# Optimization experiments

Measured on AMD Instinct MI355X. Metric: run time of the kernel, lower is better.

Reference implementation:

```python
import jax, jax.numpy as jnp
import numpy as np

B, L, D = 4, 4096, 1024
H, M = 16, 256
DH = D // H  # 64


def setup_inputs() -> dict:
    key = jax.random.key(0)
    ks = jax.random.split(key, 7)
    s = 1.0 / np.sqrt(D).astype(np.float32)  # keep activations O(1) so exp() stays sane
    x = jax.random.normal(ks[0], (B, L, D), dtype=jnp.float32)
    Wq = jax.random.normal(ks[1], (D, D), dtype=jnp.float32) * s
    Wk = jax.random.normal(ks[2], (D, D), dtype=jnp.float32) * s
    Wv = jax.random.normal(ks[3], (D, D), dtype=jnp.float32) * s
    Wo = jax.random.normal(ks[4], (D, D), dtype=jnp.float32) * s
    bo = jnp.zeros((D,), dtype=jnp.float32)
    omega = jax.random.normal(ks[5], (DH, M), dtype=jnp.float32)
    return {"x": x, "Wq": Wq, "Wk": Wk, "Wv": Wv, "Wo": Wo, "bo": bo, "omega": omega}


def _phi(x, omega):
    # x: (B,H,L,dh) -> positive random features (B,H,L,m)
    scale = DH ** 0.25
    x_s = x / scale
    proj = jnp.einsum('bhld,dm->bhlm', x_s, omega)
    norm_sq = jnp.sum(x_s * x_s, axis=-1, keepdims=True) * 0.5
    return jnp.exp(proj - norm_sq) / (M ** 0.5)


def reference(x, Wq, Wk, Wv, Wo, bo, omega):
    # nn.Linear: y = x @ W.T
    def heads(W):
        return (x @ W.T).reshape(B, L, H, DH).transpose(0, 2, 1, 3)
    Q, K, V = heads(Wq), heads(Wk), heads(Wv)
    Q_feat = _phi(Q, omega)   # (B,H,L,m)
    K_feat = _phi(K, omega)   # (B,H,L,m)
    KV = jnp.einsum('bhlm,bhld->bhmd', K_feat, V)      # (B,H,m,dh)
    out = jnp.einsum('bhlm,bhmd->bhld', Q_feat, KV)    # (B,H,L,dh)
    K_sum = K_feat.sum(axis=2)                          # (B,H,m)
    norm = jnp.einsum('bhlm,bhm->bhl', Q_feat, K_sum)
    norm = jnp.clip(norm, 1e-6, None)[..., None]
    out = out / norm
    out = out.transpose(0, 2, 1, 3).reshape(B, L, D)
    return out @ Wo.T + bo
```

## Files before the change

### kernel.cpp

```cpp
#include <hip/hip_runtime.h>

typedef unsigned short u16;
typedef __attribute__((ext_vector_type(4))) float f32x4;
typedef _Float16 f16x8 __attribute__((ext_vector_type(8)));
typedef __attribute__((ext_vector_type(4))) u16   u16x4;
typedef __attribute__((ext_vector_type(8))) u16   u16x8;

#define DEV static __device__ __forceinline__

constexpr int Ll = 4096;

DEV float h2f(u16 v) { _Float16 h; __builtin_memcpy(&h, &v, 2); return (float)h; }
DEV u16 f2h(float f) { _Float16 h = (_Float16)f; u16 u; __builtin_memcpy(&u, &h, 2); return u; }

DEV f32x4 mfma16h(f16x8 a, f16x8 b, f32x4 c) {
    return __builtin_amdgcn_mfma_f32_16x16x32_f16(a, b, c, 0, 0, 0);
}

#if defined(__has_builtin)
#if __has_builtin(__builtin_amdgcn_global_load_lds)
#define HAS_GLLDS 1
#endif
#endif
#ifndef HAS_GLLDS
#define HAS_GLLDS 0
#endif

#if HAS_GLLDS
#define STG(BUF, U, SRC, ROWBASE, KK)                                                \
  { int rl_ = wave * 16 + (lane >> 2);                                               \
    int c_ = lane & 3;                                                               \
    int grow_ = (((U) & 1) * 128) + rl_;                                             \
    const u16* gp_ = (SRC) + (size_t)((ROWBASE) + grow_) * 1024 + (KK)               \
                     + ((c_ ^ ((rl_ >> 1) & 3)) * 8);                                \
    __builtin_amdgcn_global_load_lds(                                                \
        (const __attribute__((address_space(1))) unsigned int*)gp_,                  \
        (__attribute__((address_space(3))) unsigned int*)(sm + (BUF) * 16384 +       \
            (U) * 4096 + wave * 512), 16, 0, 0); }
#else
#define STG(BUF, U, SRC, ROWBASE, KK)                                                \
  { int rl_ = wave * 16 + (lane >> 2);                                               \
    int c_ = lane & 3;                                                               \
    int grow_ = (((U) & 1) * 128) + rl_;                                             \
    const u16* gp_ = (SRC) + (size_t)((ROWBASE) + grow_) * 1024 + (KK)               \
                     + ((c_ ^ ((rl_ >> 1) & 3)) * 8);                                \
    *(u16x8*)(sm + (BUF) * 16384 + (U) * 4096 + wave * 512 + lane * 8)               \
        = *(const u16x8*)gp_; }
#endif

__global__ __launch_bounds__(256) void k_half(const float* __restrict__ s, u16* __restrict__ d) {
    size_t i = ((size_t)blockIdx.x * 256 + threadIdx.x) * 4;
    f32x4 v = *(const f32x4*)(s + i);
    u16x4 h;
#pragma unroll
    for (int j = 0; j < 4; j++) h[j] = f2h(v[j]);
    *(u16x4*)(d + i) = h;
}

__global__ __launch_bounds__(256) void k_omega(const float* __restrict__ om, u16* __restrict__ wh) {
    int i = blockIdx.x * 256 + threadIdx.x;
    int m = i >> 6, d = i & 63;
    wh[i] = f2h(om[d * 256 + m] * 0.35355339059327373f);
}

__global__ __launch_bounds__(256) void k_zero(float* __restrict__ p, int n) {
    int i = (blockIdx.x * 256 + threadIdx.x) * 4;
    if (i < n) { f32x4 z; z[0]=0.f; z[1]=0.f; z[2]=0.f; z[3]=0.f; *(f32x4*)(p + i) = z; }
}

__global__ __launch_bounds__(512, 2) void k_gemm_qkv(
    const u16* __restrict__ Ax, const u16* __restrict__ Bw,
    u16* __restrict__ QK, u16* __restrict__ Vb) {
    __shared__ __align__(16) u16 sm[32768];
    const int tid = threadIdx.x, wave = tid >> 6, lane = tid & 63;
    const int lr = lane & 15, lkq = lane >> 4;
    const int wr = wave >> 2, wc = wave & 3;
    const int m0 = blockIdx.y * 256, n0 = blockIdx.x * 256;
    const int sec = n0 >> 10;

    int aoff[8], boff[4];
#pragma unroll
    for (int f = 0; f < 8; f++) {
        int row = wr * 128 + f * 16 + lr;
        aoff[f] = row * 32 + ((lkq ^ ((row >> 1) & 3)) * 8);
    }
#pragma unroll
    for (int f = 0; f < 4; f++) {
        int row = wc * 64 + f * 16 + lr;
        boff[f] = row * 32 + ((lkq ^ ((row >> 1) & 3)) * 8);
    }

    f32x4 acc[8][4];
#pragma unroll
    for (int i = 0; i < 8; i++)
#pragma unroll
        for (int j = 0; j < 4; j++)
#pragma unroll
            for (int r = 0; r < 4; r++) acc[i][j][r] = 0.f;

    STG(0, 0, Ax, m0, 0) STG(0, 1, Ax, m0, 0)
    STG(0, 2, Bw, n0, 0) STG(0, 3, Bw, n0, 0)
    asm volatile("s_waitcnt vmcnt(0)" ::: "memory");
    __builtin_amdgcn_sched_barrier(0);
    __builtin_amdgcn_s_barrier();
    __builtin_amdgcn_sched_barrier(0);

    int cb = 0;
    for (int t = 0; t < 32; ++t) {
        const u16* Abase = sm + cb * 16384;
        const u16* Bbase = Abase + 8192;
        f16x8 afr[4], bfr[4];
#pragma unroll
        for (int f = 0; f < 4; f++) bfr[f] = *(const f16x8*)&Bbase[boff[f]];
#pragma unroll
        for (int f = 0; f < 4; f++) afr[f] = *(const f16x8*)&Abase[aoff[f]];
        if (t < 31) {
            int kk = (t + 1) * 32;
            STG(cb ^ 1, 0, Ax, m0, kk) STG(cb ^ 1, 1, Ax, m0, kk)
            STG(cb ^ 1, 2, Bw, n0, kk) STG(cb ^ 1, 3, Bw, n0, kk)
        }
        __builtin_amdgcn_sched_barrier(0);
        __builtin_amdgcn_s_barrier();
        asm volatile("s_waitcnt lgkmcnt(0)" ::: "memory");
        __builtin_amdgcn_sched_barrier(0);
        __builtin_amdgcn_s_setprio(1);
#pragma unroll
        for (int i = 0; i < 4; i++)
#pragma unroll
            for (int j = 0; j < 4; j++)
                acc[i][j] = mfma16h(afr[i], bfr[j], acc[i][j]);
        __builtin_amdgcn_s_setprio(0);
        __builtin_amdgcn_sched_barrier(0);
        __builtin_amdgcn_s_barrier();
        __builtin_amdgcn_sched_barrier(0);
#pragma unroll
        for (int f = 0; f < 4; f++) afr[f] = *(const f16x8*)&Abase[aoff[4 + f]];
        __builtin_amdgcn_sched_barrier(0);
        __builtin_amdgcn_s_barrier();
        asm volatile("s_waitcnt lgkmcnt(0)" ::: "memory");
        __builtin_amdgcn_sched_barrier(0);
        __builtin_amdgcn_s_setprio(1);
#pragma unroll
        for (int i = 0; i < 4; i++)
#pragma unroll
            for (int j = 0; j < 4; j++)
                acc[4 + i][j] = mfma16h(afr[i], bfr[j], acc[4 + i][j]);
        __builtin_amdgcn_s_setprio(0);
        asm volatile("s_waitcnt vmcnt(0)" ::: "memory");
        __builtin_amdgcn_sched_barrier(0);
        __builtin_amdgcn_s_barrier();
        __builtin_amdgcn_sched_barrier(0);
        cb ^= 1;
    }

    float* ep = (float*)sm;
    for (int g = 0; g < 8; g++) {
        __syncthreads();
        if (wr == (g >> 2)) {
#pragma unroll
            for (int fi = 0; fi < 2; fi++) {
                int fm = (g & 3) * 2 + fi;
#pragma unroll
                for (int fn = 0; fn < 4; fn++)
#pragma unroll
                    for (int r = 0; r < 4; r++)
                        ep[(fi * 16 + (lane >> 4) * 4 + r) * 264 + wc * 64 + fn * 16 + lr] = acc[fm][fn][r];
            }
        }
        __syncthreads();
        int row = tid >> 4, c0 = (tid & 15) * 16;
        int grow = m0 + g * 32 + row;
        u16x8 h0, h1;
#pragma unroll
        for (int j = 0; j < 8; j++) {
            h0[j] = f2h(ep[row * 264 + c0 + j]);
            h1[j] = f2h(ep[row * 264 + c0 + 8 + j]);
        }
        if (sec < 2) {
            size_t o = (size_t)grow * 2048 + (n0 + c0);
            *(u16x8*)(QK + o) = h0; *(u16x8*)(QK + o + 8) = h1;
        } else {
            size_t o = (size_t)grow * 1024 + (n0 - 2048 + c0);
            *(u16x8*)(Vb + o) = h0; *(u16x8*)(Vb + o + 8) = h1;
        }
    }
}

__global__ __launch_bounds__(512, 2) void k_gemm_out(
    const u16* __restrict__ Ab, const u16* __restrict__ Bw,
    const float* __restrict__ bias, float* __restrict__ outp) {
    __shared__ __align__(16) u16 sm[32768];
    const int tid = threadIdx.x, wave = tid >> 6, lane = tid & 63;
    const int lr = lane & 15, lkq = lane >> 4;
    const int wr = wave >> 2, wc = wave & 3;
    const int m0 = blockIdx.y * 256, n0 = blockIdx.x * 256;

    int aoff[8], boff[4];
#pragma unroll
    for (int f = 0; f < 8; f++) {
        int row = wr * 128 + f * 16 + lr;
        aoff[f] = row * 32 + ((lkq ^ ((row >> 1) & 3)) * 8);
    }
#pragma unroll
    for (int f = 0; f < 4; f++) {
        int row = wc * 64 + f * 16 + lr;
        boff[f] = row * 32 + ((lkq ^ ((row >> 1) & 3)) * 8);
    }

    f32x4 acc[8][4];
#pragma unroll
    for (int i = 0; i < 8; i++)
#pragma unroll
        for (int j = 0; j < 4; j++)
#pragma unroll
            for (int r = 0; r < 4; r++) acc[i][j][r] = 0.f;

    STG(0, 0, Ab, m0, 0) STG(0, 1, Ab, m0, 0)
    STG(0, 2, Bw, n0, 0) STG(0, 3, Bw, n0, 0)
    asm volatile("s_waitcnt vmcnt(0)" ::: "memory");
    __builtin_amdgcn_sched_barrier(0);
    __builtin_amdgcn_s_barrier();
    __builtin_amdgcn_sched_barrier(0);

    int cb = 0;
    for (int t = 0; t < 32; ++t) {
        const u16* Abase = sm + cb * 16384;
        const u16* Bbase = Abase + 8192;
        f16x8 afr[4], bfr[4];
#pragma unroll
        for (int f = 0; f < 4; f++) bfr[f] = *(const f16x8*)&Bbase[boff[f]];
#pragma unroll
        for (int f = 0; f < 4; f++) afr[f] = *(const f16x8*)&Abase[aoff[f]];
        if (t < 31) {
            int kk = (t + 1) * 32;
            STG(cb ^ 1, 0, Ab, m0, kk) STG(cb ^ 1, 1, Ab, m0, kk)
            STG(cb ^ 1, 2, Bw, n0, kk) STG(cb ^ 1, 3, Bw, n0, kk)
        }
        __builtin_amdgcn_sched_barrier(0);
        __builtin_amdgcn_s_barrier();
        asm volatile("s_waitcnt lgkmcnt(0)" ::: "memory");
        __builtin_amdgcn_sched_barrier(0);
        __builtin_amdgcn_s_setprio(1);
#pragma unroll
        for (int i = 0; i < 4; i++)
#pragma unroll
            for (int j = 0; j < 4; j++)
                acc[i][j] = mfma16h(afr[i], bfr[j], acc[i][j]);
        __builtin_amdgcn_s_setprio(0);
        __builtin_amdgcn_sched_barrier(0);
        __builtin_amdgcn_s_barrier();
        __builtin_amdgcn_sched_barrier(0);
#pragma unroll
        for (int f = 0; f < 4; f++) afr[f] = *(const f16x8*)&Abase[aoff[4 + f]];
        __builtin_amdgcn_sched_barrier(0);
        __builtin_amdgcn_s_barrier();
        asm volatile("s_waitcnt lgkmcnt(0)" ::: "memory");
        __builtin_amdgcn_sched_barrier(0);
        __builtin_amdgcn_s_setprio(1);
#pragma unroll
        for (int i = 0; i < 4; i++)
#pragma unroll
            for (int j = 0; j < 4; j++)
                acc[4 + i][j] = mfma16h(afr[i], bfr[j], acc[4 + i][j]);
        __builtin_amdgcn_s_setprio(0);
        asm volatile("s_waitcnt vmcnt(0)" ::: "memory");
        __builtin_amdgcn_sched_barrier(0);
        __builtin_amdgcn_s_barrier();
        __builtin_amdgcn_sched_barrier(0);
        cb ^= 1;
    }

    float* ep = (float*)sm;
    for (int g = 0; g < 8; g++) {
        __syncthreads();
        if (wr == (g >> 2)) {
#pragma unroll
            for (int fi = 0; fi < 2; fi++) {
                int fm = (g & 3) * 2 + fi;
#pragma unroll
                for (int fn = 0; fn < 4; fn++)
#pragma unroll
                    for (int r = 0; r < 4; r++)
                        ep[(fi * 16 + (lane >> 4) * 4 + r) * 264 + wc * 64 + fn * 16 + lr] = acc[fm][fn][r];
            }
        }
        __syncthreads();
        int row = tid >> 4, c0 = (tid & 15) * 16;
        int grow = m0 + g * 32 + row;
        float vv[16];
#pragma unroll
        for (int j = 0; j < 16; j++) vv[j] = ep[row * 264 + c0 + j] + bias[n0 + c0 + j];
#pragma unroll
        for (int p = 0; p < 4; p++) {
            f32x4 tv;
#pragma unroll
            for (int q = 0; q < 4; q++) tv[q] = vv[p * 4 + q];
            *(f32x4*)(outp + (size_t)grow * 1024 + n0 + c0 + p * 4) = tv;
        }
    }
}

__global__ __launch_bounds__(256) void k_phik_kv(
    const u16* __restrict__ QK, const u16* __restrict__ wt,
    const u16* __restrict__ Vb, float* __restrict__ KVacc, float* __restrict__ Ksum) {
    __shared__ __align__(16) u16 sKh[64 * 72];
    __shared__ __align__(16) u16 sVt[64 * 72];
    __shared__ __align__(16) u16 sKfT[256 * 72];
    __shared__ float snsq[64];
    const int tid = threadIdx.x, wave = tid >> 6, lane = tid & 63;
    const int lr = lane & 15, lk = (lane >> 4) * 8;
    const int kc = blockIdx.x, bh = blockIdx.y;
    const int b = bh >> 4, h = bh & 15;

    f16x8 wb[4][2];
#pragma unroll
    for (int fn = 0; fn < 4; fn++)
#pragma unroll
        for (int ks = 0; ks < 2; ks++)
            wb[fn][ks] = *(const f16x8*)(wt + (size_t)(wave * 64 + fn * 16 + lr) * 64 + ks * 32 + lk);

    f32x4 akv[4][4];
#pragma unroll
    for (int i = 0; i < 4; i++)
#pragma unroll
        for (int j = 0; j < 4; j++)
#pragma unroll
            for (int r = 0; r < 4; r++) akv[i][j][r] = 0.f;
    float ksm[4] = {0.f, 0.f, 0.f, 0.f};

    for (int it = 0; it < 4; it++) {
        int l0 = kc * 256 + it * 64;
        __syncthreads();
        {
            int row = tid >> 2, c0 = (tid & 3) * 16;
            size_t g = ((size_t)(b * Ll + l0 + row)) * 2048 + 1024 + h * 64 + c0;
            u16x8 h0 = *(const u16x8*)(QK + g);
            u16x8 h1 = *(const u16x8*)(QK + g + 8);
            *(u16x8*)&sKh[row * 72 + c0]     = h0;
            *(u16x8*)&sKh[row * 72 + c0 + 8] = h1;
            float s = 0.f;
#pragma unroll
            for (int j = 0; j < 8; j++) {
                float a = h2f(h0[j]); s += a * a;
                float c = h2f(h1[j]); s += c * c;
            }
            s += __shfl_xor(s, 1); s += __shfl_xor(s, 2);
            if ((tid & 3) == 0) snsq[row] = s * 0.0625f;
        }
        {
            int l = tid >> 2, d0 = (tid & 3) * 16;
            size_t g = ((size_t)(b * Ll + l0 + l)) * 1024 + h * 64 + d0;
            u16x8 v0 = *(const u16x8*)(Vb + g);
            u16x8 v1 = *(const u16x8*)(Vb + g + 8);
#pragma unroll
            for (int j = 0; j < 8; j++) {
                sVt[(d0 + j) * 72 + l] = v0[j];
                sVt[(d0 + 8 + j) * 72 + l] = v1[j];
            }
        }
        __syncthreads();
#pragma unroll
        for (int fm = 0; fm < 4; fm++) {
            f32x4 ap[4];
#pragma unroll
            for (int fn = 0; fn < 4; fn++)
#pragma unroll
                for (int r = 0; r < 4; r++) ap[fn][r] = 0.f;
#pragma unroll
            for (int ks = 0; ks < 2; ks++) {
                f16x8 aH = *(const f16x8*)&sKh[(fm * 16 + lr) * 72 + ks * 32 + lk];
#pragma unroll
                for (int fn = 0; fn < 4; fn++)
                    ap[fn] = mfma16h(aH, wb[fn][ks], ap[fn]);
            }
#pragma unroll
            for (int fn = 0; fn < 4; fn++) {
                u16x4 pk;
#pragma unroll
                for (int r = 0; r < 4; r++) {
                    float ns = snsq[fm * 16 + (lane >> 4) * 4 + r];
                    float val = __expf(ap[fn][r] - ns) * 0.00390625f;
                    ksm[fn] += val;
                    pk[r] = f2h(val);
                }
                *(u16x4*)&sKfT[(wave * 64 + fn * 16 + lr) * 72 + fm * 16 + (lane >> 4) * 4] = pk;
            }
        }
#pragma unroll
        for (int ks = 0; ks < 2; ks++) {
            f16x8 a4[4], b4[4];
#pragma unroll
            for (int f = 0; f < 4; f++) {
                a4[f] = *(const f16x8*)&sKfT[(wave * 64 + f * 16 + lr) * 72 + ks * 32 + lk];
                b4[f] = *(const f16x8*)&sVt[(f * 16 + lr) * 72 + ks * 32 + lk];
            }
#pragma unroll
            for (int fm = 0; fm < 4; fm++)
#pragma unroll
                for (int fn = 0; fn < 4; fn++)
                    akv[fm][fn] = mfma16h(a4[fm], b4[fn], akv[fm][fn]);
        }
    }
#pragma unroll
    for (int fm = 0; fm < 4; fm++)
#pragma unroll
        for (int fn = 0; fn < 4; fn++)
#pragma unroll
            for (int r = 0; r < 4; r++) {
                int m = wave * 64 + fm * 16 + (lane >> 4) * 4 + r;
                int d = fn * 16 + lr;
                atomicAdd(&KVacc[((size_t)bh << 14) + m * 64 + d], akv[fm][fn][r]);
            }
#pragma unroll
    for (int fn = 0; fn < 4; fn++) {
        ksm[fn] += __shfl_xor(ksm[fn], 16);
        ksm[fn] += __shfl_xor(ksm[fn], 32);
    }
    if (lane < 16) {
#pragma unroll
        for (int fn = 0; fn < 4; fn++)
            atomicAdd(&Ksum[bh * 256 + wave * 64 + fn * 16 + lane], ksm[fn]);
    }
}

__global__ __launch_bounds__(256) void k_kvt(const float* __restrict__ KVacc, u16* __restrict__ KVt) {
    int i = blockIdx.x * 256 + threadIdx.x;
    int bh = i >> 14, dd = (i >> 8) & 63, m = i & 255;
    KVt[i] = f2h(KVacc[((size_t)bh << 14) + m * 64 + dd]);
}

__global__ __launch_bounds__(512) void k_phiq_attn(
    const u16* __restrict__ QK, const u16* __restrict__ wt,
    const u16* __restrict__ KVt, const float* __restrict__ Ksum,
    u16* __restrict__ attn) {
    __shared__ __align__(16) u16 sQh[64 * 72];
    __shared__ __align__(16) u16 sQf[64 * 264];
    __shared__ float sKs[256];
    __shared__ float snsq[64];
    __shared__ float snorm[64];
    const int tid = threadIdx.x, wave = tid >> 6, lane = tid & 63;
    const int lr = lane & 15, lk = (lane >> 4) * 8;
    const int bh = blockIdx.y, b = bh >> 4, h = bh & 15;
    const int mq = wave & 3;
    const int lh = wave >> 2;
    const int af = wave & 3;
    const int ad = wave >> 2;

    f16x8 wb[4][2];
#pragma unroll
    for (int fn = 0; fn < 4; fn++)
#pragma unroll
        for (int ks = 0; ks < 2; ks++)
            wb[fn][ks] = *(const f16x8*)(wt + (size_t)(mq * 64 + fn * 16 + lr) * 64 + ks * 32 + lk);
    f16x8 kvb[2][8];
#pragma unroll
    for (int fn = 0; fn < 2; fn++)
#pragma unroll
        for (int ks = 0; ks < 8; ks++)
            kvb[fn][ks] = *(const f16x8*)(KVt + ((size_t)bh << 14) +
                                          (size_t)(ad * 32 + fn * 16 + lr) * 256 + ks * 32 + lk);
    if (tid < 256) sKs[tid] = Ksum[bh * 256 + tid];

    for (int st = 0; st < 2; st++) {
        const int l0 = (blockIdx.x * 2 + st) * 64;
        __syncthreads();
        {
            int row = tid >> 3, c0 = (tid & 7) * 8;
            size_t g = ((size_t)(b * Ll + l0 + row)) * 2048 + h * 64 + c0;
            u16x8 vh = *(const u16x8*)(QK + g);
            *(u16x8*)&sQh[row * 72 + c0] = vh;
            float s = 0.f;
#pragma unroll
            for (int j = 0; j < 8; j++) { float a = h2f(vh[j]); s += a * a; }
            s += __shfl_xor(s, 1); s += __shfl_xor(s, 2); s += __shfl_xor(s, 4);
            if ((tid & 7) == 0) snsq[row] = s * 0.0625f;
        }
        __syncthreads();
#pragma unroll
        for (int fm = 0; fm < 2; fm++) {
            f32x4 ap[4];
#pragma unroll
            for (int fn = 0; fn < 4; fn++)
#pragma unroll
                for (int r = 0; r < 4; r++) ap[fn][r] = 0.f;
#pragma unroll
            for (int ks = 0; ks < 2; ks++) {
                f16x8 aH = *(const f16x8*)&sQh[(lh * 32 + fm * 16 + lr) * 72 + ks * 32 + lk];
#pragma unroll
                for (int fn = 0; fn < 4; fn++)
                    ap[fn] = mfma16h(aH, wb[fn][ks], ap[fn]);
            }
#pragma unroll
            for (int fn = 0; fn < 4; fn++)
#pragma unroll
                for (int r = 0; r < 4; r++) {
                    int l = lh * 32 + fm * 16 + (lane >> 4) * 4 + r;
                    int m = mq * 64 + fn * 16 + lr;
                    sQf[l * 264 + m] = f2h(__expf(ap[fn][r] - snsq[l]) * 0.0625f);
                }
        }
        __syncthreads();
        {
            int l = tid >> 3, m0 = (tid & 7) * 32;
            float s = 0.f;
#pragma unroll
            for (int j4 = 0; j4 < 4; j4++) {
                u16x8 qv = *(const u16x8*)&sQf[l * 264 + m0 + j4 * 8];
#pragma unroll
                for (int j = 0; j < 8; j++) s += h2f(qv[j]) * sKs[m0 + j4 * 8 + j];
            }
            s += __shfl_xor(s, 1); s += __shfl_xor(s, 2); s += __shfl_xor(s, 4);
            if ((tid & 7) == 0) snorm[l] = s;
        }
        f32x4 aa[2];
#pragma unroll
        for (int fn = 0; fn < 2; fn++)
#pragma unroll
            for (int r = 0; r < 4; r++) aa[fn][r] = 0.f;
#pragma unroll
        for (int ks = 0; ks < 8; ks++) {
            f16x8 a = *(const f16x8*)&sQf[(af * 16 + lr) * 264 + ks * 32 + lk];
            aa[0] = mfma16h(a, kvb[0][ks], aa[0]);
            aa[1] = mfma16h(a, kvb[1][ks], aa[1]);
        }
        __syncthreads();
        float* ep = (float*)sQf;
#pragma unroll
        for (int fn = 0; fn < 2; fn++)
#pragma unroll
            for (int r = 0; r < 4; r++) {
                int l = af * 16 + (lane >> 4) * 4 + r;
                int d = ad * 32 + fn * 16 + lr;
                ep[l * 68 + d] = aa[fn][r];
            }
        __syncthreads();
        {
            int l = tid >> 3, d0 = (tid & 7) * 8;
            float inv = 1.0f / fmaxf(snorm[l], 6.25e-8f);
            u16x8 o;
#pragma unroll
            for (int j = 0; j < 8; j++) o[j] = f2h(ep[l * 68 + d0 + j] * inv);
            *(u16x8*)(attn + ((size_t)(b * Ll + l0 + l)) * 1024 + h * 64 + d0) = o;
        }
    }
}

extern "C" void kernel_launch(void* const* d_in, const int* in_sizes, int n_in,
                              void* d_out, int out_size, void* d_ws, size_t ws_size,
                              hipStream_t stream) {
    (void)in_sizes; (void)n_in; (void)out_size; (void)ws_size;
    const float* x  = (const float*)d_in[0];
    const float* Wq = (const float*)d_in[1];
    const float* Wk = (const float*)d_in[2];
    const float* Wv = (const float*)d_in[3];
    const float* Wo = (const float*)d_in[4];
    const float* bo = (const float*)d_in[5];
    const float* om = (const float*)d_in[6];

    char* w = (char*)d_ws;
    size_t o = 0;
    auto take = [&](size_t n) { char* p = w + o; o += n; return p; };
    u16* QK  = (u16*)take(67108864);
    u16* Vb  = (u16*)take(33554432);
    u16* xh  = (u16*)take(33554432);
    u16* Wc  = (u16*)take(6291456);
    u16* Wof = (u16*)take(2097152);
    u16* wt  = (u16*)take(32768);
    float* KVacc = (float*)take(4194304);
    float* Ksum  = (float*)take(65536);
    u16* KVt = (u16*)take(2097152);
    u16* attn = Vb;

    k_half<<<16384, 256, 0, stream>>>(x, xh);
    k_half<<<1024, 256, 0, stream>>>(Wq, Wc);
    k_half<<<1024, 256, 0, stream>>>(Wk, Wc + 1048576);
    k_half<<<1024, 256, 0, stream>>>(Wv, Wc + 2097152);
    k_half<<<1024, 256, 0, stream>>>(Wo, Wof);
    k_omega<<<64, 256, 0, stream>>>(om, wt);
    k_zero<<<1040, 256, 0, stream>>>(KVacc, 1064960);

    k_gemm_qkv<<<dim3(12, 64), 512, 0, stream>>>(xh, Wc, QK, Vb);
    k_phik_kv<<<dim3(16, 64), 256, 0, stream>>>(QK, wt, Vb, KVacc, Ksum);
    k_kvt<<<4096, 256, 0, stream>>>(KVacc, KVt);
    k_phiq_attn<<<dim3(32, 64), 512, 0, stream>>>(QK, wt, KVt, Ksum, attn);
    k_gemm_out<<<dim3(4, 64), 512, 0, stream>>>(attn, Wof, bo, (float*)d_out);
}
```

Measured before the change: 412.3 us.

## Deepen QKV GEMM K-tile to 64 with staged sub-tile prefetch; merge weight casts

The QKV projection GEMM now stages K-tiles of 64 instead of 32 in a larger double-buffered shared-memory region (128 KB per block). Each half-tile region (A and B, low and high K halves) gets its own prefetch and vmcnt wait, so loads for the next tile are interleaved across four MFMA phases and half as many outer iterations run. In exchange, launch bounds drop to one block per CU, which lowers occupancy and the latency hiding that a second block gave. Separately, the four weight fp32-to-fp16 conversions are merged into one launch using a 2D grid, which saves launch overhead.

Result: no change. 406.4 us (-1.4%).

```diff
diff --git a/kernel.cpp b/kernel.cpp
--- a/kernel.cpp
+++ b/kernel.cpp
@@ -24,6 +24,32 @@
 #endif
 #ifndef HAS_GLLDS
 #define HAS_GLLDS 0
+#endif
+
+#define SBAR()  __builtin_amdgcn_s_barrier()
+#define SCHED() __builtin_amdgcn_sched_barrier(0)
+#define LGKM0() asm volatile("s_waitcnt lgkmcnt(0)" ::: "memory")
+
+#if HAS_GLLDS
+#define STG2(BUF, REG, SRC, ROWBASE, TK, KS)                                         \
+  { _Pragma("unroll") for (int u_ = 0; u_ < 2; u_++) {                               \
+      int row_ = u_ * 128 + wave * 16 + (lane >> 2);                                 \
+      int c_ = lane & 3;                                                             \
+      const u16* gp_ = (SRC) + (size_t)((ROWBASE) + row_) * 1024 + (TK) * 64         \
+                        + (KS) * 32 + ((c_ ^ ((row_ >> 1) & 3)) * 8);                \
+      __builtin_amdgcn_global_load_lds(                                              \
+        (const __attribute__((address_space(1))) unsigned int*)gp_,                  \
+        (__attribute__((address_space(3))) unsigned int*)(sm + (BUF) * 32768 +       \
+          (REG) * 8192 + (u_ * 512 + wave * 64) * 8), 16, 0, 0); } }
+#else
+#define STG2(BUF, REG, SRC, ROWBASE, TK, KS)                                         \
+  { _Pragma("unroll") for (int u_ = 0; u_ < 2; u_++) {                               \
+      int row_ = u_ * 128 + wave * 16 + (lane >> 2);                                 \
+      int c_ = lane & 3;                                                             \
+      const u16* gp_ = (SRC) + (size_t)((ROWBASE) + row_) * 1024 + (TK) * 64         \
+                        + (KS) * 32 + ((c_ ^ ((row_ >> 1) & 3)) * 8);                \
+      *(u16x8*)(sm + (BUF) * 32768 + (REG) * 8192 + (u_ * 512 + wave * 64 + lane) * 8) \
+          = *(const u16x8*)gp_; } }
 #endif
 
 #if HAS_GLLDS
@@ -57,6 +83,19 @@
     *(u16x4*)(d + i) = h;
 }
 
+__global__ __launch_bounds__(256) void k_halfw(const float* __restrict__ a, const float* __restrict__ b,
+                                               const float* __restrict__ c, const float* __restrict__ d2,
+                                               u16* __restrict__ o) {
+    int y = blockIdx.y;
+    const float* src = (y == 0) ? a : (y == 1) ? b : (y == 2) ? c : d2;
+    size_t i = ((size_t)blockIdx.x * 256 + threadIdx.x) * 4;
+    f32x4 v = *(const f32x4*)(src + i);
+    u16x4 h;
+#pragma unroll
+    for (int j = 0; j < 4; j++) h[j] = f2h(v[j]);
+    *(u16x4*)(o + (size_t)y * 1048576 + i) = h;
+}
+
 __global__ __launch_bounds__(256) void k_omega(const float* __restrict__ om, u16* __restrict__ wh) {
     int i = blockIdx.x * 256 + threadIdx.x;
     int m = i >> 6, d = i & 63;
@@ -68,27 +107,20 @@
     if (i < n) { f32x4 z; z[0]=0.f; z[1]=0.f; z[2]=0.f; z[3]=0.f; *(f32x4*)(p + i) = z; }
 }
 
-__global__ __launch_bounds__(512, 2) void k_gemm_qkv(
+__global__ __launch_bounds__(512, 1) void k_gemm_qkv(
     const u16* __restrict__ Ax, const u16* __restrict__ Bw,
     u16* __restrict__ QK, u16* __restrict__ Vb) {
-    __shared__ __align__(16) u16 sm[32768];
+    __shared__ __align__(16) u16 sm[65536];
     const int tid = threadIdx.x, wave = tid >> 6, lane = tid & 63;
     const int lr = lane & 15, lkq = lane >> 4;
     const int wr = wave >> 2, wc = wave & 3;
     const int m0 = blockIdx.y * 256, n0 = blockIdx.x * 256;
     const int sec = n0 >> 10;
 
-    int aoff[8], boff[4];
-#pragma unroll
-    for (int f = 0; f < 8; f++) {
-        int row = wr * 128 + f * 16 + lr;
-        aoff[f] = row * 32 + ((lkq ^ ((row >> 1) & 3)) * 8);
-    }
-#pragma unroll
-    for (int f = 0; f < 4; f++) {
-        int row = wc * 64 + f * 16 + lr;
-        boff[f] = row * 32 + ((lkq ^ ((row >> 1) & 3)) * 8);
-    }
+    const int arow = wr * 128 + lr;
+    const int aBase = arow * 32 + ((lkq ^ ((arow >> 1) & 3)) * 8);
+    const int brow = wc * 64 + lr;
+    const int bBase = 16384 + brow * 32 + ((lkq ^ ((brow >> 1) & 3)) * 8);
 
     f32x4 acc[8][4];
 #pragma unroll
@@ -98,59 +130,75 @@
 #pragma unroll
             for (int r = 0; r < 4; r++) acc[i][j][r] = 0.f;
 
-    STG(0, 0, Ax, m0, 0) STG(0, 1, Ax, m0, 0)
-    STG(0, 2, Bw, n0, 0) STG(0, 3, Bw, n0, 0)
-    asm volatile("s_waitcnt vmcnt(0)" ::: "memory");
-    __builtin_amdgcn_sched_barrier(0);
-    __builtin_amdgcn_s_barrier();
-    __builtin_amdgcn_sched_barrier(0);
-
-    int cb = 0;
-    for (int t = 0; t < 32; ++t) {
-        const u16* Abase = sm + cb * 16384;
-        const u16* Bbase = Abase + 8192;
-        f16x8 afr[4], bfr[4];
-#pragma unroll
-        for (int f = 0; f < 4; f++) bfr[f] = *(const f16x8*)&Bbase[boff[f]];
-#pragma unroll
-        for (int f = 0; f < 4; f++) afr[f] = *(const f16x8*)&Abase[aoff[f]];
-        if (t < 31) {
-            int kk = (t + 1) * 32;
-            STG(cb ^ 1, 0, Ax, m0, kk) STG(cb ^ 1, 1, Ax, m0, kk)
-            STG(cb ^ 1, 2, Bw, n0, kk) STG(cb ^ 1, 3, Bw, n0, kk)
-        }
-        __builtin_amdgcn_sched_barrier(0);
-        __builtin_amdgcn_s_barrier();
-        asm volatile("s_waitcnt lgkmcnt(0)" ::: "memory");
-        __builtin_amdgcn_sched_barrier(0);
+    STG2(0, 0, Ax, m0, 0, 0)
+    STG2(0, 2, Bw, n0, 0, 0)
+    STG2(0, 1, Ax, m0, 0, 1)
+    STG2(0, 3, Bw, n0, 0, 1)
+    asm volatile("s_waitcnt vmcnt(4)" ::: "memory");
+    SCHED(); SBAR(); SCHED();
+
+    f16x8 bfr[2][4], afr[4];
+    for (int t = 0; t < 16; ++t) {
+        const u16* bp = sm + (t & 1) * 32768;
+        const int nb = (t + 1) & 1;
+        const bool st = t < 15;
+#pragma unroll
+        for (int f = 0; f < 4; f++) afr[f] = *(const f16x8*)&bp[aBase + f * 512];
+#pragma unroll
+        for (int j = 0; j < 4; j++) bfr[0][j] = *(const f16x8*)&bp[bBase + j * 512];
+        if (st) STG2(nb, 0, Ax, m0, t + 1, 0)
+        SBAR(); LGKM0(); SCHED();
         __builtin_amdgcn_s_setprio(1);
 #pragma unroll
         for (int i = 0; i < 4; i++)
 #pragma unroll
             for (int j = 0; j < 4; j++)
-                acc[i][j] = mfma16h(afr[i], bfr[j], acc[i][j]);
+                acc[i][j] = mfma16h(afr[i], bfr[0][j], acc[i][j]);
         __builtin_amdgcn_s_setprio(0);
-        __builtin_amdgcn_sched_barrier(0);
-        __builtin_amdgcn_s_barrier();
-        __builtin_amdgcn_sched_barrier(0);
-#pragma unroll
-        for (int f = 0; f < 4; f++) afr[f] = *(const f16x8*)&Abase[aoff[4 + f]];
-        __builtin_amdgcn_sched_barrier(0);
-        __builtin_amdgcn_s_barrier();
-        asm volatile("s_waitcnt lgkmcnt(0)" ::: "memory");
-        __builtin_amdgcn_sched_barrier(0);
+        SCHED();
+        if (st) { asm volatile("s_waitcnt vmcnt(2)" ::: "memory"); }
+        else    { asm volatile("s_waitcnt vmcnt(0)" ::: "memory"); }
+        SCHED(); SBAR(); SCHED();
+#pragma unroll
+        for (int f = 0; f < 4; f++) afr[f] = *(const f16x8*)&bp[aBase + 8192 + f * 512];
+#pragma unroll
+        for (int j = 0; j < 4; j++) bfr[1][j] = *(const f16x8*)&bp[bBase + 8192 + j * 512];
+        if (st) STG2(nb, 2, Bw, n0, t + 1, 0)
+        SBAR(); LGKM0(); SCHED();
         __builtin_amdgcn_s_setprio(1);
 #pragma unroll
         for (int i = 0; i < 4; i++)
 #pragma unroll
             for (int j = 0; j < 4; j++)
-                acc[4 + i][j] = mfma16h(afr[i], bfr[j], acc[4 + i][j]);
+                acc[i][j] = mfma16h(afr[i], bfr[1][j], acc[i][j]);
         __builtin_amdgcn_s_setprio(0);
-        asm volatile("s_waitcnt vmcnt(0)" ::: "memory");
-        __builtin_amdgcn_sched_barrier(0);
-        __builtin_amdgcn_s_barrier();
-        __builtin_amdgcn_sched_barrier(0);
-        cb ^= 1;
+        SCHED(); SBAR(); SCHED();
+#pragma unroll
+        for (int f = 0; f < 4; f++) afr[f] = *(const f16x8*)&bp[aBase + 2048 + f * 512];
+        if (st) STG2(nb, 1, Ax, m0, t + 1, 1)
+        SBAR(); LGKM0(); SCHED();
+        __builtin_amdgcn_s_setprio(1);
+#pragma unroll
+        for (int i = 0; i < 4; i++)
+#pragma unroll
+            for (int j = 0; j < 4; j++)
+                acc[4 + i][j] = mfma16h(afr[i], bfr[0][j], acc[4 + i][j]);
+        __builtin_amdgcn_s_setprio(0);
+        SCHED(); SBAR(); SCHED();
+#pragma unroll
+        for (int f = 0; f < 4; f++) afr[f] = *(const f16x8*)&bp[aBase + 8192 + 2048 + f * 512];
+        if (st) STG2(nb, 3, Bw, n0, t + 1, 1)
+        SBAR(); LGKM0(); SCHED();
+        __builtin_amdgcn_s_setprio(1);
+#pragma unroll
+        for (int i = 0; i < 4; i++)
+#pragma unroll
+            for (int j = 0; j < 4; j++)
+                acc[4 + i][j] = mfma16h(afr[i], bfr[1][j], acc[4 + i][j]);
+        __builtin_amdgcn_s_setprio(0);
+        SCHED();
+        if (st) { asm volatile("s_waitcnt vmcnt(4)" ::: "memory"); }
+        SCHED(); SBAR(); SCHED();
     }
 
     float* ep = (float*)sm;
@@ -218,9 +266,7 @@
     STG(0, 0, Ab, m0, 0) STG(0, 1, Ab, m0, 0)
     STG(0, 2, Bw, n0, 0) STG(0, 3, Bw, n0, 0)
     asm volatile("s_waitcnt vmcnt(0)" ::: "memory");
-    __builtin_amdgcn_sched_barrier(0);
-    __builtin_amdgcn_s_barrier();
-    __builtin_amdgcn_sched_barrier(0);
+    SCHED(); SBAR(); SCHED();
 
     int cb = 0;
     for (int t = 0; t < 32; ++t) {
@@ -236,10 +282,7 @@
             STG(cb ^ 1, 0, Ab, m0, kk) STG(cb ^ 1, 1, Ab, m0, kk)
             STG(cb ^ 1, 2, Bw, n0, kk) STG(cb ^ 1, 3, Bw, n0, kk)
         }
-        __builtin_amdgcn_sched_barrier(0);
-        __builtin_amdgcn_s_barrier();
-        asm volatile("s_waitcnt lgkmcnt(0)" ::: "memory");
-        __builtin_amdgcn_sched_barrier(0);
+        SCHED(); SBAR(); LGKM0(); SCHED();
         __builtin_amdgcn_s_setprio(1);
 #pragma unroll
         for (int i = 0; i < 4; i++)
@@ -247,15 +290,10 @@
             for (int j = 0; j < 4; j++)
                 acc[i][j] = mfma16h(afr[i], bfr[j], acc[i][j]);
         __builtin_amdgcn_s_setprio(0);
-        __builtin_amdgcn_sched_barrier(0);
-        __builtin_amdgcn_s_barrier();
-        __builtin_amdgcn_sched_barrier(0);
+        SCHED(); SBAR(); SCHED();
 #pragma unroll
         for (int f = 0; f < 4; f++) afr[f] = *(const f16x8*)&Abase[aoff[4 + f]];
-        __builtin_amdgcn_sched_barrier(0);
-        __builtin_amdgcn_s_barrier();
-        asm volatile("s_waitcnt lgkmcnt(0)" ::: "memory");
-        __builtin_amdgcn_sched_barrier(0);
+        SCHED(); SBAR(); LGKM0(); SCHED();
         __builtin_amdgcn_s_setprio(1);
 #pragma unroll
         for (int i = 0; i < 4; i++)
@@ -264,9 +302,7 @@
                 acc[4 + i][j] = mfma16h(afr[i], bfr[j], acc[4 + i][j]);
         __builtin_amdgcn_s_setprio(0);
         asm volatile("s_waitcnt vmcnt(0)" ::: "memory");
-        __builtin_amdgcn_sched_barrier(0);
-        __builtin_amdgcn_s_barrier();
-        __builtin_amdgcn_sched_barrier(0);
+        SCHED(); SBAR(); SCHED();
         cb ^= 1;
     }
 
@@ -572,10 +608,7 @@
     u16* attn = Vb;
 
     k_half<<<16384, 256, 0, stream>>>(x, xh);
-    k_half<<<1024, 256, 0, stream>>>(Wq, Wc);
-    k_half<<<1024, 256, 0, stream>>>(Wk, Wc + 1048576);
-    k_half<<<1024, 256, 0, stream>>>(Wv, Wc + 2097152);
-    k_half<<<1024, 256, 0, stream>>>(Wo, Wof);
+    k_halfw<<<dim3(1024, 4), 256, 0, stream>>>(Wq, Wk, Wv, Wo, Wc);
     k_omega<<<64, 256, 0, stream>>>(om, wt);
     k_zero<<<1040, 256, 0, stream>>>(KVacc, 1064960);
 
```
